# Performance work log

Measured on AMD Instinct MI355X. Metric: run time of the kernel, lower is better.

Reference implementation:

```python
import jax, jax.numpy as jnp
import numpy as np

B, K, DIM = 8192, 256, 1024


def setup_inputs() -> dict:
    key = jax.random.key(0)
    k1, k2, k3 = jax.random.split(key, 3)
    x = jax.random.normal(k1, (B, DIM), dtype=jnp.float32)
    centers = jax.random.uniform(k2, (K, DIM), dtype=jnp.float32)
    # torch init: D = 0.2 * rand + 0.9
    D = 0.2 * jax.random.uniform(k3, (K, DIM), dtype=jnp.float32) + 0.9
    return {"x": x, "centers": centers, "D": D}


def reference(x, centers, D):
    # Per-class axis-aligned (diagonal) covariance
    D_abs = jnp.abs(D) + 1e-4                      # [K, DIM]
    D_inv = 1.0 / D_abs                            # [K, DIM]
    log_det = jnp.sum(jnp.log(D_abs), axis=1)      # [K]
    det_scale_factor = -0.5 * log_det
    det_scale_safe = jnp.exp(det_scale_factor - jnp.max(det_scale_factor))  # [K]

    # dist_sq[b,k] = sum_d (x[b,d]-c[k,d])^2 * D_inv[k,d]
    # Expanded quadratic form avoids materializing the [B,K,DIM] diff tensor.
    x2 = jnp.einsum('bd,kd->bk', x * x, D_inv)             # [B, K]
    xc = jnp.einsum('bd,kd->bk', x, centers * D_inv)       # [B, K]
    c2 = jnp.sum(centers * centers * D_inv, axis=1)        # [K]
    dist_sq = x2 - 2.0 * xc + c2[None, :]                  # [B, K]

    # Gaussian path (isCauchy=False)
    expo = -0.5 * dist_sq
    expo_safe = expo - jnp.max(expo, axis=-1, keepdims=True)
    numer_safe = det_scale_safe[None, :] * jnp.exp(expo_safe)
    denom_safe = jnp.sum(numer_safe, axis=1, keepdims=True)
    resp = numer_safe / denom_safe                         # [B, K]
    return resp
```

## Files before the change

kernel.cpp:

```cpp
#include <hip/hip_runtime.h>

typedef _Float16 f16x8 __attribute__((ext_vector_type(8)));
typedef _Float16 f16x4 __attribute__((ext_vector_type(4)));
typedef float f32x4 __attribute__((ext_vector_type(4)));

#define B_N 8192
#define K_N 256
#define DIM_N 1024

__global__ __launch_bounds__(256) void prep_w(const float* __restrict__ Dm,
                                              const float* __restrict__ Cm,
                                              _Float16* __restrict__ Upk,
                                              _Float16* __restrict__ Wpk,
                                              float* __restrict__ ec) {
    const int k = blockIdx.x, t = threadIdx.x;
    const int d = t * 4;
    const float4 dv = *(const float4*)(Dm + (size_t)k * DIM_N + d);
    const float4 cv = *(const float4*)(Cm + (size_t)k * DIM_N + d);
    float dd[4] = {dv.x, dv.y, dv.z, dv.w};
    float cc[4] = {cv.x, cv.y, cv.z, cv.w};
    f16x4 uo, wo;
    float llog = 0.f, lc2 = 0.f;
#pragma unroll
    for (int i = 0; i < 4; ++i) {
        float da = fabsf(dd[i]) + 1e-4f;
        float dinv = 1.0f / da;
        llog += logf(da);
        lc2 += cc[i] * cc[i] * dinv;
        uo[i] = (_Float16)(dinv - 1.0f);
        wo[i] = (_Float16)(-2.0f * cc[i] * dinv);
    }
    const int cg = k >> 4, cl = k & 15;
    const int kc = d >> 5, g = (d >> 3) & 3, j0 = d & 7;
    const size_t off = ((size_t)(cg * 32 + kc) * 64 + g * 16 + cl) * 8 + j0;
    *(f16x4*)(Upk + off) = uo;
    *(f16x4*)(Wpk + off) = wo;
    float both = llog + lc2;
#pragma unroll
    for (int m = 1; m <= 32; m <<= 1) both += __shfl_xor(both, m, 64);
    __shared__ float sb[4];
    if ((t & 63) == 0) sb[t >> 6] = both;
    __syncthreads();
    if (t == 0) ec[k] = -0.5f * (sb[0] + sb[1] + sb[2] + sb[3]);
}

__global__ __launch_bounds__(512, 1)
void gmm_fused(const float* __restrict__ x,
               const _Float16* __restrict__ Upk,
               const _Float16* __restrict__ Wpk,
               const float* __restrict__ ecg,
               float* __restrict__ out) {
    __shared__ __align__(16) char lds[16384];
    __shared__ float red[8][32];

    const int tid = threadIdx.x;
    const int wave = tid >> 6, lane = tid & 63;
    const int l15 = lane & 15, g4 = lane >> 4;
    const int bRow = blockIdx.x * 32;

    const int srow = tid >> 4, sdg = tid & 15;
    const float* xp = x + (size_t)(bRow + srow) * DIM_N + sdg * 4;
    const int wByte = srow * 128 + ((((sdg >> 1) ^ (srow & 7)) << 4) | ((sdg & 1) << 3));

    const _Float16* upb = Upk + (size_t)(wave * 2) * 32 * 512 + lane * 8;
    const _Float16* wpb = Wpk + (size_t)(wave * 2) * 32 * 512 + lane * 8;

    int aRd[2][2];
#pragma unroll
    for (int m = 0; m < 2; ++m)
#pragma unroll
        for (int k2 = 0; k2 < 2; ++k2) {
            const int row = m * 16 + l15;
            aRd[m][k2] = row * 128 + ((((k2 * 4 + g4) ^ (row & 7)) << 4));
        }

    f32x4 acc[2][2];
#pragma unroll
    for (int m = 0; m < 2; ++m)
#pragma unroll
        for (int n = 0; n < 2; ++n) { f32x4 z = {0.f, 0.f, 0.f, 0.f}; acc[m][n] = z; }

    float4 xv[6];
    f16x8 ub[2][2][2], wb[2][2][2];

    auto issueX = [&](int slot, int c) { xv[slot] = *(const float4*)(xp + c * 64); };
    auto issueB = [&](int bank, int c) {
#pragma unroll
        for (int n = 0; n < 2; ++n)
#pragma unroll
            for (int k2 = 0; k2 < 2; ++k2) {
                const int kc = c * 2 + k2;
                ub[bank][n][k2] = *(const f16x8*)(upb + (size_t)(n * 32 + kc) * 512);
                wb[bank][n][k2] = *(const f16x8*)(wpb + (size_t)(n * 32 + kc) * 512);
            }
    };
    auto stage = [&](int sel, int slot) {
        char* base = lds + sel * 8192;
        const float f0 = xv[slot].x, f1 = xv[slot].y, f2 = xv[slot].z, f3 = xv[slot].w;
        f16x4 h2 = {(_Float16)(f0 * f0), (_Float16)(f1 * f1),
                    (_Float16)(f2 * f2), (_Float16)(f3 * f3)};
        f16x4 hx = {(_Float16)f0, (_Float16)f1, (_Float16)f2, (_Float16)f3};
        *(f16x4*)(base + wByte) = h2;
        *(f16x4*)(base + 4096 + wByte) = hx;
    };
    auto compute = [&](int sel, int bank) {
        char* base = lds + sel * 8192;
        f16x8 a2f[2][2], axf[2][2];
#pragma unroll
        for (int m = 0; m < 2; ++m)
#pragma unroll
            for (int k2 = 0; k2 < 2; ++k2) {
                a2f[m][k2] = *(const f16x8*)(base + aRd[m][k2]);
                axf[m][k2] = *(const f16x8*)(base + 4096 + aRd[m][k2]);
            }
        __builtin_amdgcn_s_setprio(1);
#pragma unroll
        for (int m = 0; m < 2; ++m)
#pragma unroll
            for (int n = 0; n < 2; ++n)
#pragma unroll
                for (int k2 = 0; k2 < 2; ++k2) {
                    acc[m][n] = __builtin_amdgcn_mfma_f32_16x16x32_f16(a2f[m][k2], ub[bank][n][k2], acc[m][n], 0, 0, 0);
                    acc[m][n] = __builtin_amdgcn_mfma_f32_16x16x32_f16(axf[m][k2], wb[bank][n][k2], acc[m][n], 0, 0, 0);
                }
        __builtin_amdgcn_s_setprio(0);
    };

    issueB(0, 0);
    issueB(1, 1);
#pragma unroll
    for (int s = 0; s < 6; ++s) issueX(s, s);
    stage(0, 0);
    asm volatile("s_waitcnt lgkmcnt(0)" ::: "memory");
    __builtin_amdgcn_s_barrier();
    __builtin_amdgcn_sched_barrier(0);

#pragma unroll
    for (int c = 0; c < 16; ++c) {
        const int sel = c & 1;
        if (c < 10) issueX(c % 6, c + 6);
        if (c < 15) stage(sel ^ 1, (c + 1) % 6);
        compute(sel, sel);
        if (c < 14) issueB(sel, c + 2);
        if (c < 15) {
            asm volatile("s_waitcnt lgkmcnt(0)" ::: "memory");
            __builtin_amdgcn_s_barrier();
            __builtin_amdgcn_sched_barrier(0);
        }
    }

    const int cls0 = wave * 32 + l15;
    const float ecv[2] = {ecg[cls0], ecg[cls0 + 16]};

    float e[2][2][4];
#pragma unroll
    for (int m = 0; m < 2; ++m)
#pragma unroll
        for (int n = 0; n < 2; ++n)
#pragma unroll
            for (int j = 0; j < 4; ++j)
                e[m][n][j] = fmaf(-0.5f, acc[m][n][j], ecv[n]);

    float mx[2][4];
#pragma unroll
    for (int m = 0; m < 2; ++m)
#pragma unroll
        for (int j = 0; j < 4; ++j) mx[m][j] = fmaxf(e[m][0][j], e[m][1][j]);
#pragma unroll
    for (int msk = 1; msk <= 8; msk <<= 1)
#pragma unroll
        for (int m = 0; m < 2; ++m)
#pragma unroll
            for (int j = 0; j < 4; ++j)
                mx[m][j] = fmaxf(mx[m][j], __shfl_xor(mx[m][j], msk, 64));
    if (l15 == 0) {
#pragma unroll
        for (int m = 0; m < 2; ++m)
#pragma unroll
            for (int j = 0; j < 4; ++j) red[wave][m * 16 + g4 * 4 + j] = mx[m][j];
    }
    __syncthreads();
    float gm[2][4];
#pragma unroll
    for (int m = 0; m < 2; ++m)
#pragma unroll
        for (int j = 0; j < 4; ++j) {
            const int r = m * 16 + g4 * 4 + j;
            float v = red[0][r];
#pragma unroll
            for (int w = 1; w < 8; ++w) v = fmaxf(v, red[w][r]);
            gm[m][j] = v;
        }
    __syncthreads();

    float p[2][2][4], sm[2][4];
#pragma unroll
    for (int m = 0; m < 2; ++m)
#pragma unroll
        for (int j = 0; j < 4; ++j) sm[m][j] = 0.f;
#pragma unroll
    for (int m = 0; m < 2; ++m)
#pragma unroll
        for (int n = 0; n < 2; ++n)
#pragma unroll
            for (int j = 0; j < 4; ++j) {
                p[m][n][j] = __expf(e[m][n][j] - gm[m][j]);
                sm[m][j] += p[m][n][j];
            }
#pragma unroll
    for (int msk = 1; msk <= 8; msk <<= 1)
#pragma unroll
        for (int m = 0; m < 2; ++m)
#pragma unroll
            for (int j = 0; j < 4; ++j) sm[m][j] += __shfl_xor(sm[m][j], msk, 64);
    if (l15 == 0) {
#pragma unroll
        for (int m = 0; m < 2; ++m)
#pragma unroll
            for (int j = 0; j < 4; ++j) red[wave][m * 16 + g4 * 4 + j] = sm[m][j];
    }
    __syncthreads();
#pragma unroll
    for (int m = 0; m < 2; ++m)
#pragma unroll
        for (int j = 0; j < 4; ++j) {
            const int r = m * 16 + g4 * 4 + j;
            float t = red[0][r];
#pragma unroll
            for (int w = 1; w < 8; ++w) t += red[w][r];
            const float inv = 1.0f / t;
#pragma unroll
            for (int n = 0; n < 2; ++n)
                out[(size_t)(bRow + r) * K_N + cls0 + n * 16] = p[m][n][j] * inv;
        }
}

extern "C" void kernel_launch(void* const* d_in, const int* in_sizes, int n_in,
                              void* d_out, int out_size, void* d_ws, size_t ws_size,
                              hipStream_t stream) {
    const float* x = (const float*)d_in[0];
    const float* cen = (const float*)d_in[1];
    const float* Dm = (const float*)d_in[2];
    float* out = (float*)d_out;

    char* ws = (char*)d_ws;
    _Float16* Upk = (_Float16*)(ws);
    _Float16* Wpk = (_Float16*)(ws + 524288);
    float* ec = (float*)(ws + 1048576);

    prep_w<<<dim3(K_N), dim3(256), 0, stream>>>(Dm, cen, Upk, Wpk, ec);
    gmm_fused<<<dim3(B_N / 32), dim3(512), 0, stream>>>(x, Upk, Wpk, ec, out);
}
```

Baseline: 31.79 us.

## Stage two K-chunks per LDS buffer to halve barriers; drop setprio

The LDS staging buffer doubles so each double-buffer half holds two 64-wide K chunks, and the main loop runs 8 iterations instead of 16 with one barrier per pair of chunks. Between the two computes of an iteration it reissues B-fragment loads into the bank that was just consumed. This cuts workgroup barrier and waitcnt stalls and removes the s_setprio raise around the MFMA block. The costs are more LDS per block, which may not matter at one block per CU, and more staging work front-loaded before each compute.

Result: faster. 30.67 us (-3.5%).

```diff
diff --git a/kernel.cpp b/kernel.cpp
--- a/kernel.cpp
+++ b/kernel.cpp
@@ -50,7 +50,7 @@
                const _Float16* __restrict__ Wpk,
                const float* __restrict__ ecg,
                float* __restrict__ out) {
-    __shared__ __align__(16) char lds[16384];
+    __shared__ __align__(16) char lds[32768];
     __shared__ float red[8][32];
 
     const int tid = threadIdx.x;
@@ -94,26 +94,25 @@
                 wb[bank][n][k2] = *(const f16x8*)(wpb + (size_t)(n * 32 + kc) * 512);
             }
     };
-    auto stage = [&](int sel, int slot) {
-        char* base = lds + sel * 8192;
+    auto stage1 = [&](int buf, int sub, int slot) {
+        char* base = lds + buf * 16384 + sub * 4096;
         const float f0 = xv[slot].x, f1 = xv[slot].y, f2 = xv[slot].z, f3 = xv[slot].w;
         f16x4 h2 = {(_Float16)(f0 * f0), (_Float16)(f1 * f1),
                     (_Float16)(f2 * f2), (_Float16)(f3 * f3)};
         f16x4 hx = {(_Float16)f0, (_Float16)f1, (_Float16)f2, (_Float16)f3};
         *(f16x4*)(base + wByte) = h2;
-        *(f16x4*)(base + 4096 + wByte) = hx;
+        *(f16x4*)(base + 8192 + wByte) = hx;
     };
-    auto compute = [&](int sel, int bank) {
-        char* base = lds + sel * 8192;
+    auto compute = [&](int buf, int sub, int bank) {
+        char* base = lds + buf * 16384 + sub * 4096;
         f16x8 a2f[2][2], axf[2][2];
 #pragma unroll
         for (int m = 0; m < 2; ++m)
 #pragma unroll
             for (int k2 = 0; k2 < 2; ++k2) {
                 a2f[m][k2] = *(const f16x8*)(base + aRd[m][k2]);
-                axf[m][k2] = *(const f16x8*)(base + 4096 + aRd[m][k2]);
+                axf[m][k2] = *(const f16x8*)(base + 8192 + aRd[m][k2]);
             }
-        __builtin_amdgcn_s_setprio(1);
 #pragma unroll
         for (int m = 0; m < 2; ++m)
 #pragma unroll
@@ -123,26 +122,28 @@
                     acc[m][n] = __builtin_amdgcn_mfma_f32_16x16x32_f16(a2f[m][k2], ub[bank][n][k2], acc[m][n], 0, 0, 0);
                     acc[m][n] = __builtin_amdgcn_mfma_f32_16x16x32_f16(axf[m][k2], wb[bank][n][k2], acc[m][n], 0, 0, 0);
                 }
-        __builtin_amdgcn_s_setprio(0);
     };
 
     issueB(0, 0);
     issueB(1, 1);
 #pragma unroll
     for (int s = 0; s < 6; ++s) issueX(s, s);
-    stage(0, 0);
+    stage1(0, 0, 0);
+    stage1(0, 1, 1);
     asm volatile("s_waitcnt lgkmcnt(0)" ::: "memory");
     __builtin_amdgcn_s_barrier();
     __builtin_amdgcn_sched_barrier(0);
 
 #pragma unroll
-    for (int c = 0; c < 16; ++c) {
-        const int sel = c & 1;
-        if (c < 10) issueX(c % 6, c + 6);
-        if (c < 15) stage(sel ^ 1, (c + 1) % 6);
-        compute(sel, sel);
-        if (c < 14) issueB(sel, c + 2);
-        if (c < 15) {
+    for (int p = 0; p < 8; ++p) {
+        const int buf = p & 1, nbuf = buf ^ 1;
+        if (p < 5) { issueX((2 * p) % 6, 2 * p + 6); issueX((2 * p + 1) % 6, 2 * p + 7); }
+        if (p < 7) { stage1(nbuf, 0, (2 * p + 2) % 6); stage1(nbuf, 1, (2 * p + 3) % 6); }
+        compute(buf, 0, 0);
+        if (p < 7) issueB(0, 2 * p + 2);
+        compute(buf, 1, 1);
+        if (p < 7) issueB(1, 2 * p + 3);
+        if (p < 7) {
             asm volatile("s_waitcnt lgkmcnt(0)" ::: "memory");
             __builtin_amdgcn_s_barrier();
             __builtin_amdgcn_sched_barrier(0);
@@ -193,7 +194,7 @@
         }
     __syncthreads();
 
-    float p[2][2][4], sm[2][4];
+    float p2[2][2][4], sm[2][4];
 #pragma unroll
     for (int m = 0; m < 2; ++m)
 #pragma unroll
@@ -204,8 +205,8 @@
         for (int n = 0; n < 2; ++n)
 #pragma unroll
             for (int j = 0; j < 4; ++j) {
-                p[m][n][j] = __expf(e[m][n][j] - gm[m][j]);
-                sm[m][j] += p[m][n][j];
+                p2[m][n][j] = __expf(e[m][n][j] - gm[m][j]);
+                sm[m][j] += p2[m][n][j];
             }
 #pragma unroll
     for (int msk = 1; msk <= 8; msk <<= 1)
@@ -231,7 +232,7 @@
             const float inv = 1.0f / t;
 #pragma unroll
             for (int n = 0; n < 2; ++n)
-                out[(size_t)(bRow + r) * K_N + cls0 + n * 16] = p[m][n][j] * inv;
+                out[(size_t)(bRow + r) * K_N + cls0 + n * 16] = p2[m][n][j] * inv;
         }
 }
 
```

## Halve row tile, stage whole x tile in LDS once, square in-register

Applied to the files above, without the earlier changes.

The block row tile shrinks from 32 to 16 rows and the grid doubles to 512 blocks. The double-buffered x staging with per-chunk barriers is replaced by a single upfront load of the whole 16x1024 x tile into LDS as fp16, in the MFMA A-fragment layout. x^2 is now computed in registers from the fp16 x values rather than from fp32. Occupancy hints rise to 4 blocks per CU, which removes the barriers from the main loop and improves latency hiding. The cost is that each weight fragment is reused by half as many rows, doubling total weight traffic, and squaring in fp16 slightly changes precision.

Result: slower. 36.39 us (+14.5%).

```diff
diff --git a/kernel.cpp b/kernel.cpp
--- a/kernel.cpp
+++ b/kernel.cpp
@@ -44,46 +44,32 @@
     if (t == 0) ec[k] = -0.5f * (sb[0] + sb[1] + sb[2] + sb[3]);
 }
 
-__global__ __launch_bounds__(512, 1)
+__global__ __launch_bounds__(512, 4)
 void gmm_fused(const float* __restrict__ x,
                const _Float16* __restrict__ Upk,
                const _Float16* __restrict__ Wpk,
                const float* __restrict__ ecg,
                float* __restrict__ out) {
-    __shared__ __align__(16) char lds[16384];
-    __shared__ float red[8][32];
+    __shared__ __align__(16) char xlds[32768];
+    __shared__ float red[8][16];
 
     const int tid = threadIdx.x;
     const int wave = tid >> 6, lane = tid & 63;
     const int l15 = lane & 15, g4 = lane >> 4;
-    const int bRow = blockIdx.x * 32;
+    const int bRow = blockIdx.x * 16;
 
-    const int srow = tid >> 4, sdg = tid & 15;
-    const float* xp = x + (size_t)(bRow + srow) * DIM_N + sdg * 4;
-    const int wByte = srow * 128 + ((((sdg >> 1) ^ (srow & 7)) << 4) | ((sdg & 1) << 3));
+    const int sr = tid & 15, sq = tid >> 4;
+    const float* xq = x + (size_t)(bRow + sr) * DIM_N + sq * 32;
+    const int wbase = (sq >> 1) * 2048 + (sq & 1) * 1024 + sr * 16;
 
     const _Float16* upb = Upk + (size_t)(wave * 2) * 32 * 512 + lane * 8;
     const _Float16* wpb = Wpk + (size_t)(wave * 2) * 32 * 512 + lane * 8;
 
-    int aRd[2][2];
-#pragma unroll
-    for (int m = 0; m < 2; ++m)
-#pragma unroll
-        for (int k2 = 0; k2 < 2; ++k2) {
-            const int row = m * 16 + l15;
-            aRd[m][k2] = row * 128 + ((((k2 * 4 + g4) ^ (row & 7)) << 4));
-        }
+    f32x4 acc[2];
+    { f32x4 z = {0.f, 0.f, 0.f, 0.f}; acc[0] = z; acc[1] = z; }
 
-    f32x4 acc[2][2];
-#pragma unroll
-    for (int m = 0; m < 2; ++m)
-#pragma unroll
-        for (int n = 0; n < 2; ++n) { f32x4 z = {0.f, 0.f, 0.f, 0.f}; acc[m][n] = z; }
-
-    float4 xv[6];
     f16x8 ub[2][2][2], wb[2][2][2];
 
-    auto issueX = [&](int slot, int c) { xv[slot] = *(const float4*)(xp + c * 64); };
     auto issueB = [&](int bank, int c) {
 #pragma unroll
         for (int n = 0; n < 2; ++n)
@@ -94,145 +80,105 @@
                 wb[bank][n][k2] = *(const f16x8*)(wpb + (size_t)(n * 32 + kc) * 512);
             }
     };
-    auto stage = [&](int sel, int slot) {
-        char* base = lds + sel * 8192;
-        const float f0 = xv[slot].x, f1 = xv[slot].y, f2 = xv[slot].z, f3 = xv[slot].w;
-        f16x4 h2 = {(_Float16)(f0 * f0), (_Float16)(f1 * f1),
-                    (_Float16)(f2 * f2), (_Float16)(f3 * f3)};
-        f16x4 hx = {(_Float16)f0, (_Float16)f1, (_Float16)f2, (_Float16)f3};
-        *(f16x4*)(base + wByte) = h2;
-        *(f16x4*)(base + 4096 + wByte) = hx;
-    };
-    auto compute = [&](int sel, int bank) {
-        char* base = lds + sel * 8192;
-        f16x8 a2f[2][2], axf[2][2];
-#pragma unroll
-        for (int m = 0; m < 2; ++m)
-#pragma unroll
-            for (int k2 = 0; k2 < 2; ++k2) {
-                a2f[m][k2] = *(const f16x8*)(base + aRd[m][k2]);
-                axf[m][k2] = *(const f16x8*)(base + 4096 + aRd[m][k2]);
-            }
-        __builtin_amdgcn_s_setprio(1);
-#pragma unroll
-        for (int m = 0; m < 2; ++m)
-#pragma unroll
-            for (int n = 0; n < 2; ++n)
-#pragma unroll
-                for (int k2 = 0; k2 < 2; ++k2) {
-                    acc[m][n] = __builtin_amdgcn_mfma_f32_16x16x32_f16(a2f[m][k2], ub[bank][n][k2], acc[m][n], 0, 0, 0);
-                    acc[m][n] = __builtin_amdgcn_mfma_f32_16x16x32_f16(axf[m][k2], wb[bank][n][k2], acc[m][n], 0, 0, 0);
-                }
-        __builtin_amdgcn_s_setprio(0);
-    };
 
     issueB(0, 0);
     issueB(1, 1);
+    {
+        float4 v[8];
 #pragma unroll
-    for (int s = 0; s < 6; ++s) issueX(s, s);
-    stage(0, 0);
-    asm volatile("s_waitcnt lgkmcnt(0)" ::: "memory");
-    __builtin_amdgcn_s_barrier();
-    __builtin_amdgcn_sched_barrier(0);
+        for (int h = 0; h < 8; ++h) v[h] = *(const float4*)(xq + h * 4);
+#pragma unroll
+        for (int hh = 0; hh < 4; ++hh) {
+            const float4 a = v[hh * 2], b = v[hh * 2 + 1];
+            f16x8 h8 = {(_Float16)a.x, (_Float16)a.y, (_Float16)a.z, (_Float16)a.w,
+                        (_Float16)b.x, (_Float16)b.y, (_Float16)b.z, (_Float16)b.w};
+            *(f16x8*)(xlds + wbase + hh * 256) = h8;
+        }
+    }
+    __syncthreads();
 
 #pragma unroll
     for (int c = 0; c < 16; ++c) {
-        const int sel = c & 1;
-        if (c < 10) issueX(c % 6, c + 6);
-        if (c < 15) stage(sel ^ 1, (c + 1) % 6);
-        compute(sel, sel);
-        if (c < 14) issueB(sel, c + 2);
-        if (c < 15) {
-            asm volatile("s_waitcnt lgkmcnt(0)" ::: "memory");
-            __builtin_amdgcn_s_barrier();
-            __builtin_amdgcn_sched_barrier(0);
+        const int bank = c & 1;
+        const char* base = xlds + c * 2048;
+        f16x8 ax0 = *(const f16x8*)(base + lane * 16);
+        f16x8 ax1 = *(const f16x8*)(base + 1024 + lane * 16);
+        const f16x8 a20 = ax0 * ax0;
+        const f16x8 a21 = ax1 * ax1;
+#pragma unroll
+        for (int n = 0; n < 2; ++n) {
+            acc[n] = __builtin_amdgcn_mfma_f32_16x16x32_f16(a20, ub[bank][n][0], acc[n], 0, 0, 0);
+            acc[n] = __builtin_amdgcn_mfma_f32_16x16x32_f16(ax0, wb[bank][n][0], acc[n], 0, 0, 0);
+            acc[n] = __builtin_amdgcn_mfma_f32_16x16x32_f16(a21, ub[bank][n][1], acc[n], 0, 0, 0);
+            acc[n] = __builtin_amdgcn_mfma_f32_16x16x32_f16(ax1, wb[bank][n][1], acc[n], 0, 0, 0);
         }
+        if (c < 14) issueB(bank, c + 2);
     }
 
     const int cls0 = wave * 32 + l15;
     const float ecv[2] = {ecg[cls0], ecg[cls0 + 16]};
 
-    float e[2][2][4];
+    float e[2][4];
 #pragma unroll
-    for (int m = 0; m < 2; ++m)
+    for (int n = 0; n < 2; ++n)
 #pragma unroll
-        for (int n = 0; n < 2; ++n)
+        for (int j = 0; j < 4; ++j)
+            e[n][j] = fmaf(-0.5f, acc[n][j], ecv[n]);
+
+    float mx[4];
 #pragma unroll
-            for (int j = 0; j < 4; ++j)
-                e[m][n][j] = fmaf(-0.5f, acc[m][n][j], ecv[n]);
-
-    float mx[2][4];
-#pragma unroll
-    for (int m = 0; m < 2; ++m)
-#pragma unroll
-        for (int j = 0; j < 4; ++j) mx[m][j] = fmaxf(e[m][0][j], e[m][1][j]);
+    for (int j = 0; j < 4; ++j) mx[j] = fmaxf(e[0][j], e[1][j]);
 #pragma unroll
     for (int msk = 1; msk <= 8; msk <<= 1)
 #pragma unroll
-        for (int m = 0; m < 2; ++m)
-#pragma unroll
-            for (int j = 0; j < 4; ++j)
-                mx[m][j] = fmaxf(mx[m][j], __shfl_xor(mx[m][j], msk, 64));
+        for (int j = 0; j < 4; ++j)
+            mx[j] = fmaxf(mx[j], __shfl_xor(mx[j], msk, 64));
     if (l15 == 0) {
 #pragma unroll
-        for (int m = 0; m < 2; ++m)
-#pragma unroll
-            for (int j = 0; j < 4; ++j) red[wave][m * 16 + g4 * 4 + j] = mx[m][j];
+        for (int j = 0; j < 4; ++j) red[wave][g4 * 4 + j] = mx[j];
     }
     __syncthreads();
-    float gm[2][4];
+    float gm[4];
 #pragma unroll
-    for (int m = 0; m < 2; ++m)
+    for (int j = 0; j < 4; ++j) {
+        const int r = g4 * 4 + j;
+        float v = red[0][r];
+#pragma unroll
+        for (int w = 1; w < 8; ++w) v = fmaxf(v, red[w][r]);
+        gm[j] = v;
+    }
+    __syncthreads();
+
+    float p2[2][4], sfs[4];
+#pragma unroll
+    for (int j = 0; j < 4; ++j) sfs[j] = 0.f;
+#pragma unroll
+    for (int n = 0; n < 2; ++n)
 #pragma unroll
         for (int j = 0; j < 4; ++j) {
-            const int r = m * 16 + g4 * 4 + j;
-            float v = red[0][r];
-#pragma unroll
-            for (int w = 1; w < 8; ++w) v = fmaxf(v, red[w][r]);
-            gm[m][j] = v;
+            p2[n][j] = __expf(e[n][j] - gm[j]);
+            sfs[j] += p2[n][j];
         }
-    __syncthreads();
-
-    float p[2][2][4], sm[2][4];
-#pragma unroll
-    for (int m = 0; m < 2; ++m)
-#pragma unroll
-        for (int j = 0; j < 4; ++j) sm[m][j] = 0.f;
-#pragma unroll
-    for (int m = 0; m < 2; ++m)
-#pragma unroll
-        for (int n = 0; n < 2; ++n)
-#pragma unroll
-            for (int j = 0; j < 4; ++j) {
-                p[m][n][j] = __expf(e[m][n][j] - gm[m][j]);
-                sm[m][j] += p[m][n][j];
-            }
 #pragma unroll
     for (int msk = 1; msk <= 8; msk <<= 1)
 #pragma unroll
-        for (int m = 0; m < 2; ++m)
-#pragma unroll
-            for (int j = 0; j < 4; ++j) sm[m][j] += __shfl_xor(sm[m][j], msk, 64);
+        for (int j = 0; j < 4; ++j) sfs[j] += __shfl_xor(sfs[j], msk, 64);
     if (l15 == 0) {
 #pragma unroll
-        for (int m = 0; m < 2; ++m)
-#pragma unroll
-            for (int j = 0; j < 4; ++j) red[wave][m * 16 + g4 * 4 + j] = sm[m][j];
+        for (int j = 0; j < 4; ++j) red[wave][g4 * 4 + j] = sfs[j];
     }
     __syncthreads();
 #pragma unroll
-    for (int m = 0; m < 2; ++m)
+    for (int j = 0; j < 4; ++j) {
+        const int r = g4 * 4 + j;
+        float t = red[0][r];
 #pragma unroll
-        for (int j = 0; j < 4; ++j) {
-            const int r = m * 16 + g4 * 4 + j;
-            float t = red[0][r];
+        for (int w = 1; w < 8; ++w) t += red[w][r];
+        const float inv = 1.0f / t;
 #pragma unroll
-            for (int w = 1; w < 8; ++w) t += red[w][r];
-            const float inv = 1.0f / t;
-#pragma unroll
-            for (int n = 0; n < 2; ++n)
-                out[(size_t)(bRow + r) * K_N + cls0 + n * 16] = p[m][n][j] * inv;
-        }
+        for (int n = 0; n < 2; ++n)
+            out[(size_t)(bRow + r) * K_N + cls0 + n * 16] = p2[n][j] * inv;
+    }
 }
 
 extern "C" void kernel_launch(void* const* d_in, const int* in_sizes, int n_in,
@@ -249,5 +195,5 @@
     float* ec = (float*)(ws + 1048576);
 
     prep_w<<<dim3(K_N), dim3(256), 0, stream>>>(Dm, cen, Upk, Wpk, ec);
-    gmm_fused<<<dim3(B_N / 32), dim3(512), 0, stream>>>(x, Upk, Wpk, ec, out);
+    gmm_fused<<<dim3(B_N / 16), dim3(512), 0, stream>>>(x, Upk, Wpk, ec, out);
 }
```
